# Optimization experiments

Hardware: AMD Instinct MI355X
Metric: run time of the kernel (lower is better)

The kernel has to match this reference:

```python
import jax, jax.numpy as jnp
import numpy as np
from jax import lax

EPS = 1e-5
NBIT = 127.0  # 8-bit symmetric: 2^(8-1)-1

def ste_round(x):
    return x + lax.stop_gradient(jnp.round(x) - x)

def quant_act(x, rng_max):
    # symmetric fake-quant of activations with learned per-cluster range
    s = rng_max / NBIT
    xq = jnp.clip(ste_round(x / s), -NBIT, NBIT) * s
    return xq, s

def fold_bn(w, gamma, beta, mean, var):
    std = jnp.sqrt(var + EPS)
    scale = gamma / std
    w_f = w * scale[:, None, None, None]
    b_f = beta - mean * scale
    return w_f, b_f

def quant_weight(w):
    # per-output-channel symmetric quant
    s = jnp.max(jnp.abs(w), axis=(1, 2, 3), keepdims=True) / NBIT
    wq = jnp.clip(ste_round(w / s), -NBIT, NBIT) * s
    return wq, s.reshape(-1)

def conv(x, w, stride=1, groups=1, pad=0):
    return lax.conv_general_dilated(
        x, w, window_strides=(stride, stride),
        padding=((pad, pad), (pad, pad)),
        dimension_numbers=('NCHW', 'OIHW', 'NCHW'),
        feature_group_count=groups)

def setup_inputs() -> dict:
    key = jax.random.key(0)
    ks = jax.random.split(key, 24)
    B, Cin, H, W = 64, 96, 28, 28
    Cmid, Cout, NC = 576, 96, 4
    d = {}
    d['x'] = jax.random.normal(ks[0], (B, Cin, H, W), dtype=jnp.float32)
    # conv1: 1x1 expansion
    d['w1'] = jax.random.normal(ks[1], (Cmid, Cin, 1, 1), jnp.float32) * 0.1
    d['g1'] = jax.random.uniform(ks[2], (Cmid,), minval=0.5, maxval=1.5)
    d['b1'] = jax.random.normal(ks[3], (Cmid,)) * 0.1
    d['m1'] = jax.random.normal(ks[4], (Cmid,)) * 0.1
    d['v1'] = jax.random.uniform(ks[5], (Cmid,), minval=0.5, maxval=1.5)
    # conv2: 3x3 depthwise
    d['w2'] = jax.random.normal(ks[6], (Cmid, 1, 3, 3), jnp.float32) * 0.1
    d['g2'] = jax.random.uniform(ks[7], (Cmid,), minval=0.5, maxval=1.5)
    d['b2'] = jax.random.normal(ks[8], (Cmid,)) * 0.1
    d['m2'] = jax.random.normal(ks[9], (Cmid,)) * 0.1
    d['v2'] = jax.random.uniform(ks[10], (Cmid,), minval=0.5, maxval=1.5)
    # conv3: 1x1 projection
    d['w3'] = jax.random.normal(ks[11], (Cout, Cmid, 1, 1), jnp.float32) * 0.1
    d['g3'] = jax.random.uniform(ks[12], (Cout,), minval=0.5, maxval=1.5)
    d['b3'] = jax.random.normal(ks[13], (Cout,)) * 0.1
    d['m3'] = jax.random.normal(ks[14], (Cout,)) * 0.1
    d['v3'] = jax.random.uniform(ks[15], (Cout,), minval=0.5, maxval=1.5)
    # per-cluster learned activation ranges for the 4 QuantAct modules
    d['r0'] = jax.random.uniform(ks[16], (NC,), minval=2.0, maxval=8.0)
    d['r1'] = jax.random.uniform(ks[17], (NC,), minval=2.0, maxval=8.0)
    d['r2'] = jax.random.uniform(ks[18], (NC,), minval=2.0, maxval=8.0)
    d['r3'] = jax.random.uniform(ks[19], (NC,), minval=2.0, maxval=8.0)
    d['cluster'] = 2
    return d

def reference(x, w1, g1, b1, m1, v1, w2, g2, b2, m2, v2,
              w3, g3, b3, m3, v3, r0, r1, r2, r3, cluster):
    identity = x  # residual path (in==out, stride==1)
    # QuantAct -> conv1 (BN-folded, per-channel quant) -> ReLU6
    xq, s0 = quant_act(x, r0[cluster])
    w1f, bf1 = fold_bn(w1, g1, b1, m1, v1)
    w1q, ws1 = quant_weight(w1f)
    y = conv(xq, w1q) + bf1[None, :, None, None]
    y = jnp.clip(y, 0.0, 6.0)
    # QuantAct1 -> depthwise conv2 -> ReLU6
    yq, s1 = quant_act(y, r1[cluster])
    w2f, bf2 = fold_bn(w2, g2, b2, m2, v2)
    w2q, ws2 = quant_weight(w2f)
    y = conv(yq, w2q, stride=1, groups=w2.shape[0], pad=1) + bf2[None, :, None, None]
    y = jnp.clip(y, 0.0, 6.0)
    # QuantAct2 -> conv3 projection
    yq, s2 = quant_act(y, r2[cluster])
    w3f, bf3 = fold_bn(w3, g3, b3, m3, v3)
    w3q, ws3 = quant_weight(w3f)
    y = conv(yq, w3q) + bf3[None, :, None, None]
    # residual add, then int32 requant
    y = y + identity
    out, s3 = quant_act(y, r3[cluster])
    return out, s3
```

## Files before the change

kernel.cpp:

```cpp
#include <hip/hip_runtime.h>
#include <cstdint>
#include <cstddef>

typedef int   v4i __attribute__((ext_vector_type(4)));
typedef float v4f __attribute__((ext_vector_type(4)));
typedef unsigned int u32;

constexpr int B_   = 64;
constexpr int CIN  = 96;
constexpr int P_   = 784;
constexpr int CMID = 576;
constexpr int COUT = 96;
constexpr int NOUT = B_ * COUT * P_;
constexpr float NBITF = 127.0f;
constexpr float EPSF  = 1e-5f;
constexpr float MAGICF = 12582912.0f;
constexpr int   BIASI  = 0x4B400000;

constexpr int XB4 = 13 * 8 * 64;
constexpr int YB4 = 13 * 36 * 64;

__device__ __forceinline__ int dot3(u32 a, u32 w, int acc) {
#if __has_builtin(__builtin_amdgcn_sdot4)
    return __builtin_amdgcn_sdot4((int)a, (int)w, acc, false);
#else
    return acc + (int)(signed char)(a)        * (int)(signed char)(w)
               + (int)(signed char)(a >> 8)   * (int)(signed char)(w >> 8)
               + (int)(signed char)(a >> 16)  * (int)(signed char)(w >> 16);
#endif
}

__device__ __forceinline__ void tr4(u32 S0, u32 S1, u32 S2, u32 S3, u32 O[4]) {
    u32 u01 = __builtin_amdgcn_perm(S1, S0, 0x05010400u);
    u32 u23 = __builtin_amdgcn_perm(S3, S2, 0x05010400u);
    u32 v01 = __builtin_amdgcn_perm(S1, S0, 0x07030602u);
    u32 v23 = __builtin_amdgcn_perm(S3, S2, 0x07030602u);
    O[0] = __builtin_amdgcn_perm(u23, u01, 0x05040100u);
    O[1] = __builtin_amdgcn_perm(u23, u01, 0x07060302u);
    O[2] = __builtin_amdgcn_perm(v23, v01, 0x05040100u);
    O[3] = __builtin_amdgcn_perm(v23, v01, 0x07060302u);
}

__device__ __forceinline__ u32 pack4(u32 t0, u32 t1, u32 t2, u32 t3) {
    u32 p01 = __builtin_amdgcn_perm(t1, t0, 0x05010400u);
    u32 p23 = __builtin_amdgcn_perm(t3, t2, 0x05010400u);
    return __builtin_amdgcn_perm(p23, p01, 0x05040100u);
}

__global__ __launch_bounds__(256)
void prep_all(const float* __restrict__ x,
              const float* __restrict__ w1, const float* __restrict__ g1,
              const float* __restrict__ b1, const float* __restrict__ m1,
              const float* __restrict__ v1,
              const float* __restrict__ w2, const float* __restrict__ g2,
              const float* __restrict__ b2, const float* __restrict__ m2,
              const float* __restrict__ v2,
              const float* __restrict__ w3, const float* __restrict__ g3,
              const float* __restrict__ b3, const float* __restrict__ m3,
              const float* __restrict__ v3,
              const float* __restrict__ r0, const float* __restrict__ r1,
              const float* __restrict__ r2, const int* __restrict__ cluster,
              u32* __restrict__ x8t2,
              int8_t* __restrict__ w1qp, float2* __restrict__ e1,
              v4i* __restrict__ w2pk,    float2* __restrict__ e2,
              int8_t* __restrict__ w3qp, float2* __restrict__ e3)
{
    __shared__ u32 T[112 * 37];
    int tid = threadIdx.x;
    int c = cluster[0];

    if (blockIdx.x < 448) {
        int pt0 = blockIdx.x % 7, b = blockIdx.x / 7;
        float inv_s0 = NBITF / r0[c];

        for (int i = tid; i < 112 * 8; i += 256) {
            int row = i >> 3, cc = 24 + (i & 7);
            T[row * 37 + cc] = 0u;
        }
        for (int u = tid; u < 24 * 28; u += 256) {
            int pq = u % 28, icq = u / 28;
            int pxb = pt0 * 112 + pq * 4;
            int q[4][4];
            #pragma unroll
            for (int j = 0; j < 4; j++) {
                v4f xv = *(const v4f*)(x + ((size_t)b * CIN + icq * 4 + j) * P_ + pxb);
                #pragma unroll
                for (int i = 0; i < 4; i++)
                    q[j][i] = (int)fminf(fmaxf(rintf(xv[i] * inv_s0), -127.f), 127.f);
            }
            #pragma unroll
            for (int i = 0; i < 4; i++) {
                u32 t0 = __builtin_amdgcn_perm((u32)q[1][i], (u32)q[0][i], 0x00000400u);
                u32 t1 = __builtin_amdgcn_perm((u32)q[3][i], (u32)q[2][i], 0x00000400u);
                T[(pq * 4 + i) * 37 + icq] = __builtin_amdgcn_perm(t1, t0, 0x05040100u);
            }
        }
        __syncthreads();
        u32* gb = x8t2 + (size_t)b * XB4 * 4;
        for (int i = tid; i < 32 * 112; i += 256) {
            int icq = i / 112, pxo = i - icq * 112;
            int px = pt0 * 112 + pxo;
            gb[(((px >> 6) * 8 + (icq >> 2)) * 64 + (px & 63)) * 4 + (icq & 3)] =
                T[pxo * 37 + icq];
        }
        return;
    }

    int lane = tid & 63, wv = tid >> 6;
    int blk = (blockIdx.x - 448) * 4 + wv;

    const float *w, *g, *bb, *mm, *vv;
    int oc, K, which;
    if (blk < CMID)            { which = 0; w = w1; g = g1; bb = b1; mm = m1; vv = v1; oc = blk;            K = CIN;  }
    else if (blk < 2 * CMID)   { which = 1; w = w2; g = g2; bb = b2; mm = m2; vv = v2; oc = blk - CMID;     K = 9;    }
    else                       { which = 2; w = w3; g = g3; bb = b3; mm = m3; vv = v3; oc = blk - 2 * CMID; K = CMID; }

    float scale = g[oc] / sqrtf(vv[oc] + EPSF);

    float mx = 0.f;
    for (int k = lane; k < K; k += 64)
        mx = fmaxf(mx, fabsf(w[oc * K + k] * scale));
    #pragma unroll
    for (int off = 1; off < 64; off <<= 1)
        mx = fmaxf(mx, __shfl_xor(mx, off));

    float s = mx / NBITF;

    int myq = 0;
    for (int k = lane; k < K; k += 64) {
        float wf = w[oc * K + k] * scale;
        float q  = fminf(fmaxf(rintf(wf / s), -127.f), 127.f);
        if (which == 0)      w1qp[oc * 144 + k] = (int8_t)q;
        else if (which == 1) myq = (int)q;
        else                 w3qp[oc * 592 + k] = (int8_t)q;
    }
    if (which == 0 && lane < 12)
        ((u32*)(w1qp + oc * 144))[24 + lane] = 0u;
    if (which == 1) {
        u32 qq[9];
        #pragma unroll
        for (int t = 0; t < 9; t++) qq[t] = (u32)__shfl(myq, t, 64) & 0xffu;
        if (lane == 0) {
            v4i pk;
            pk[0] = (int)(qq[0] | (qq[1] << 8) | (qq[2] << 16));
            pk[1] = (int)(qq[3] | (qq[4] << 8) | (qq[5] << 16));
            pk[2] = (int)(qq[6] | (qq[7] << 8) | (qq[8] << 16));
            pk[3] = 0;
            w2pk[oc] = pk;
        }
    }
    if (lane == 0) {
        float bf = bb[oc] - mm[oc] * scale;
        float s0 = r0[c] / NBITF, s1 = r1[c] / NBITF, s2 = r2[c] / NBITF;
        if (which == 0) {
            float inv_s1 = NBITF / r1[c];
            e1[oc] = make_float2(s0 * s * inv_s1, bf * inv_s1);
        } else if (which == 1) {
            float inv_s2 = NBITF / r2[c];
            e2[oc] = make_float2(s1 * s * inv_s2, bf * inv_s2);
        } else {
            e3[oc] = make_float2(s2 * s, bf);
        }
    }
}

__global__ __launch_bounds__(256)
void conv12v3(const v4i* __restrict__ x8t2, const v4i* __restrict__ w1q4,
              const float2* __restrict__ e1,
              const v4i* __restrict__ w2pk, const float2* __restrict__ e2,
              const float* __restrict__ r1, const float* __restrict__ r2,
              const int* __restrict__ cluster, v4i* __restrict__ y2t)
{
    __shared__ u32 pool[112 * 36];
    __shared__ u32 y1w[192 * 29];

    int tid = threadIdx.x, b = blockIdx.y;
    int mt = blockIdx.x / 14, rt = blockIdx.x - mt * 14;
    int R0 = 2 * rt;
    int W0 = (R0 - 1) * 28;
    int lane = tid & 63, wv = tid >> 6;
    int n = lane & 15, q4 = lane >> 4;
    int ocw = mt * 192 + wv * 48;

    int c   = cluster[0];
    int u1i = (int)fminf(rintf(6.f * NBITF / r1[c]), 127.f);
    int u2i = (int)fminf(rintf(6.f * NBITF / r2[c]), 127.f);

    const v4i* xb = x8t2 + (size_t)b * XB4;
    for (int u = tid; u < 896; u += 256) {
        int g = u / 112, pxl = u - g * 112;
        int px = min(max(W0 + pxl, 0), P_ - 1);
        v4i v = xb[((px >> 6) * 8 + g) * 64 + (px & 63)];
        *(v4i*)&pool[pxl * 36 + 4 * g] = v;
    }
    __syncthreads();

    #pragma unroll
    for (int jn = 0; jn < 3; jn++) {
        int oc  = ocw + 16 * jn + n;
        int chl = wv * 48 + 16 * jn + n;

        v4i acc[7];
        #pragma unroll
        for (int jm = 0; jm < 7; jm++) acc[jm] = (v4i){0, 0, 0, 0};

        #pragma unroll
        for (int ks = 0; ks < 2; ks++) {
            v4i bw = w1q4[oc * 9 + 4 * ks + q4];
            int g4 = (4 * ks + q4) * 4;
            #pragma unroll
            for (int jm = 0; jm < 7; jm++) {
                v4i af = *(const v4i*)&pool[(16 * jm + n) * 36 + g4];
                acc[jm] = __builtin_amdgcn_mfma_i32_16x16x64_i8(af, bw, acc[jm], 0, 0, 0);
            }
        }

        float2 e = e1[oc];
        #pragma unroll
        for (int jm = 0; jm < 7; jm++) {
            u32 t[4];
            #pragma unroll
            for (int r = 0; r < 4; r++) {
                float f = fmaf((float)acc[jm][r], e.x, e.y) + MAGICF;
                t[r] = (u32)min(max(__float_as_int(f), BIASI), BIASI + u1i);
            }
            int dw = 4 * jm + q4;
            u32 pk = pack4(t[0], t[1], t[2], t[3]);
            pk = ((unsigned)(W0 + 4 * dw) < (unsigned)P_) ? pk : 0u;
            y1w[chl * 29 + dw] = pk;
        }
    }
    __syncthreads();

    u32* y2s = pool;
    for (int u = tid; u < 384; u += 256) {
        int chl = u >> 1, orow = u & 1;
        int ch  = mt * 192 + chl;
        int rb  = chl * 29 + orow * 7;

        v4i wpk = w2pk[ch];
        u32 pk0 = (u32)wpk[0], pk1 = (u32)wpk[1], pk2 = (u32)wpk[2];
        float2 e = e2[ch];

        u32 M0 = 0, M1 = 0, M2 = 0;
        u32 D0 = y1w[rb], D1 = y1w[rb + 7], D2 = y1w[rb + 14];
        #pragma unroll
        for (int xq = 0; xq < 7; xq++) {
            u32 N0, N1, N2;
            if (xq < 6) {
                N0 = y1w[rb + xq + 1];
                N1 = y1w[rb + 7 + xq + 1];
                N2 = y1w[rb + 14 + xq + 1];
            } else { N0 = N1 = N2 = 0u; }

            int a0, a1, a2, a3;
            a0 = dot3(__builtin_amdgcn_alignbyte(D0, M0, 3), pk0, 0);
            a0 = dot3(__builtin_amdgcn_alignbyte(D1, M1, 3), pk1, a0);
            a0 = dot3(__builtin_amdgcn_alignbyte(D2, M2, 3), pk2, a0);
            a1 = dot3(D0, pk0, 0);
            a1 = dot3(D1, pk1, a1);
            a1 = dot3(D2, pk2, a1);
            a2 = dot3(__builtin_amdgcn_alignbyte(N0, D0, 1), pk0, 0);
            a2 = dot3(__builtin_amdgcn_alignbyte(N1, D1, 1), pk1, a2);
            a2 = dot3(__builtin_amdgcn_alignbyte(N2, D2, 1), pk2, a2);
            a3 = dot3(__builtin_amdgcn_alignbyte(N0, D0, 2), pk0, 0);
            a3 = dot3(__builtin_amdgcn_alignbyte(N1, D1, 2), pk1, a3);
            a3 = dot3(__builtin_amdgcn_alignbyte(N2, D2, 2), pk2, a3);

            int aa[4] = {a0, a1, a2, a3};
            u32 tq[4];
            #pragma unroll
            for (int i = 0; i < 4; i++) {
                float f = fmaf((float)aa[i], e.x, e.y) + MAGICF;
                tq[i] = (u32)min(max(__float_as_int(f), BIASI), BIASI + u2i);
            }
            y2s[chl * 15 + orow * 7 + xq] = pack4(tq[0], tq[1], tq[2], tq[3]);

            M0 = D0; M1 = D1; M2 = D2;
            D0 = N0; D1 = N1; D2 = N2;
        }
    }
    __syncthreads();

    v4i* yb = y2t + (size_t)b * YB4;
    for (int u = tid; u < 168; u += 256) {
        int kgl = u / 14, d = u - kgl * 14;
        u32 O[4][4];
        #pragma unroll
        for (int j = 0; j < 4; j++) {
            int cb = (16 * kgl + 4 * j) * 15 + d;
            tr4(y2s[cb], y2s[cb + 15], y2s[cb + 30], y2s[cb + 45], O[j]);
        }
        int gpx0 = R0 * 28 + 4 * d;
        #pragma unroll
        for (int i = 0; i < 4; i++) {
            int gp = gpx0 + i;
            v4i val = (v4i){(int)O[0][i], (int)O[1][i], (int)O[2][i], (int)O[3][i]};
            yb[((gp >> 6) * 36 + mt * 12 + kgl) * 64 + (gp & 63)] = val;
        }
    }
}

__global__ __launch_bounds__(256)
void conv3d(const v4i* __restrict__ y2t, const int8_t* __restrict__ w3qp,
            const float2* __restrict__ e3, const float* __restrict__ x,
            const float* __restrict__ r3, const int* __restrict__ cluster,
            float* __restrict__ out)
{
    int tid = threadIdx.x, b = blockIdx.y, pt = blockIdx.x;
    int lane = tid & 63, wv = tid >> 6;
    int n = lane & 15, q4 = lane >> 4;
    int pxl = wv * 16 + n;
    int px  = pt * 64 + pxl;
    int pxc = min(px, P_ - 1);

    int   c      = cluster[0];
    float s3     = r3[c] / NBITF;
    float inv_s3 = NBITF / r3[c];

    const v4i* yb  = y2t + (size_t)b * YB4;
    int pb3 = (pxc >> 6) * (36 * 64) + (pxc & 63);
    const v4i* w34 = (const v4i*)w3qp;

    v4i acc[6];
    #pragma unroll
    for (int i = 0; i < 6; i++) acc[i] = (v4i){0, 0, 0, 0};

    #pragma unroll
    for (int ks = 0; ks < 9; ks++) {
        v4i bfr = yb[pb3 + (4 * ks + q4) * 64];
        #pragma unroll
        for (int i = 0; i < 6; i++) {
            v4i afr = w34[(i * 16 + n) * 37 + 4 * ks + q4];
            acc[i] = __builtin_amdgcn_mfma_i32_16x16x64_i8(afr, bfr, acc[i], 0, 0, 0);
        }
    }

    if (px < P_) {
        #pragma unroll
        for (int i = 0; i < 6; i++) {
            #pragma unroll
            for (int r = 0; r < 4; r++) {
                int    oc = i * 16 + q4 * 4 + r;
                float2 e  = e3[oc];
                size_t gi = (size_t)(b * COUT + oc) * P_ + px;
                float v  = fmaf((float)acc[i][r], e.x, e.y) + x[gi];
                float f  = fmaf(v, inv_s3, MAGICF);
                int lvl  = min(max(__float_as_int(f) - BIASI, -127), 127);
                out[gi]  = (float)lvl * s3;
            }
        }
    }
    if (pt == 0 && b == 0 && tid == 0)
        out[NOUT] = s3;
}

extern "C" void kernel_launch(void* const* d_in, const int* in_sizes, int n_in,
                              void* d_out, int out_size, void* d_ws, size_t ws_size,
                              hipStream_t stream)
{
    const float* x  = (const float*)d_in[0];
    const float* w1 = (const float*)d_in[1];
    const float* g1 = (const float*)d_in[2];
    const float* b1 = (const float*)d_in[3];
    const float* m1 = (const float*)d_in[4];
    const float* v1 = (const float*)d_in[5];
    const float* w2 = (const float*)d_in[6];
    const float* g2 = (const float*)d_in[7];
    const float* b2 = (const float*)d_in[8];
    const float* m2 = (const float*)d_in[9];
    const float* v2 = (const float*)d_in[10];
    const float* w3 = (const float*)d_in[11];
    const float* g3 = (const float*)d_in[12];
    const float* b3 = (const float*)d_in[13];
    const float* m3 = (const float*)d_in[14];
    const float* v3 = (const float*)d_in[15];
    const float* r0 = (const float*)d_in[16];
    const float* r1 = (const float*)d_in[17];
    const float* r2 = (const float*)d_in[18];
    const float* r3 = (const float*)d_in[19];
    const int*   cl = (const int*)d_in[20];

    float* out = (float*)d_out;

    char*  ws  = (char*)d_ws;
    size_t off = 0;
    auto carve = [&](size_t bytes) {
        size_t cur = off;
        off = (off + bytes + 255) & ~(size_t)255;
        return (void*)(ws + cur);
    };
    int8_t* w1qp = (int8_t*)carve((size_t)CMID * 144);
    float2* e1   = (float2*)carve((size_t)CMID * 8);
    v4i*    w2pk = (v4i*)carve((size_t)CMID * 16);
    float2* e2   = (float2*)carve((size_t)CMID * 8);
    int8_t* w3qp = (int8_t*)carve((size_t)COUT * 592);
    float2* e3   = (float2*)carve((size_t)COUT * 8);
    u32*    x8t2 = (u32*)carve((size_t)B_ * XB4 * 16);
    v4i*    y2t  = (v4i*)carve((size_t)B_ * YB4 * 16);
    (void)ws_size; (void)in_sizes; (void)n_in; (void)out_size;

    prep_all<<<dim3(760), dim3(256), 0, stream>>>(
        x, w1, g1, b1, m1, v1, w2, g2, b2, m2, v2, w3, g3, b3, m3, v3,
        r0, r1, r2, cl, x8t2,
        w1qp, e1, w2pk, e2, w3qp, e3);

    conv12v3<<<dim3(42, B_), dim3(256), 0, stream>>>(
        (const v4i*)x8t2, (const v4i*)w1qp, e1, w2pk, e2, r1, r2, cl, y2t);

    conv3d<<<dim3(13, B_), dim3(256), 0, stream>>>(
        y2t, w3qp, e3, x, r3, cl, out);
}
```

Baseline: 174.7 us.

## Make conv1→depthwise→transpose wave-private to drop block barriers

Restructures the fused conv1/depthwise kernel so each wavefront owns its 48 channels end to end, with private LDS slices for the conv1 output and the depthwise output. This removes two block-wide __syncthreads and replaces the 256-thread strided loops with per-wave lane loops. It also reorders the MFMA loop to iterate pixels outer and channels inner, using a single accumulator per tile, and lays out the x tile as channel-group planes. The catch is more total LDS and lower lane utilisation in the depthwise and transpose stages (96 and 42 items per wave).

```diff
diff --git a/kernel.cpp b/kernel.cpp
--- a/kernel.cpp
+++ b/kernel.cpp
@@ -165,14 +165,15 @@
 }
 
 __global__ __launch_bounds__(256)
-void conv12v3(const v4i* __restrict__ x8t2, const v4i* __restrict__ w1q4,
-              const float2* __restrict__ e1,
-              const v4i* __restrict__ w2pk, const float2* __restrict__ e2,
-              const float* __restrict__ r1, const float* __restrict__ r2,
-              const int* __restrict__ cluster, v4i* __restrict__ y2t)
+void conv12w(const v4i* __restrict__ x8t2, const v4i* __restrict__ w1q4,
+             const float2* __restrict__ e1,
+             const v4i* __restrict__ w2pk, const float2* __restrict__ e2,
+             const float* __restrict__ r1, const float* __restrict__ r2,
+             const int* __restrict__ cluster, v4i* __restrict__ y2t)
 {
-    __shared__ u32 pool[112 * 36];
-    __shared__ u32 y1w[192 * 29];
+    __shared__ v4i xs4[8 * 112];
+    __shared__ u32 y1w[4][48 * 29];
+    __shared__ u32 y2s[4][48 * 15];
 
     int tid = threadIdx.x, b = blockIdx.y;
     int mt = blockIdx.x / 14, rt = blockIdx.x - mt * 14;
@@ -190,52 +191,51 @@
     for (int u = tid; u < 896; u += 256) {
         int g = u / 112, pxl = u - g * 112;
         int px = min(max(W0 + pxl, 0), P_ - 1);
-        v4i v = xb[((px >> 6) * 8 + g) * 64 + (px & 63)];
-        *(v4i*)&pool[pxl * 36 + 4 * g] = v;
+        xs4[g * 112 + pxl] = xb[((px >> 6) * 8 + g) * 64 + (px & 63)];
     }
     __syncthreads();
 
+    u32* myY1 = y1w[wv];
+    u32* myY2 = y2s[wv];
+
+    v4i    bw[3][2];
+    float2 ee[3];
     #pragma unroll
     for (int jn = 0; jn < 3; jn++) {
-        int oc  = ocw + 16 * jn + n;
-        int chl = wv * 48 + 16 * jn + n;
-
-        v4i acc[7];
-        #pragma unroll
-        for (int jm = 0; jm < 7; jm++) acc[jm] = (v4i){0, 0, 0, 0};
-
-        #pragma unroll
-        for (int ks = 0; ks < 2; ks++) {
-            v4i bw = w1q4[oc * 9 + 4 * ks + q4];
-            int g4 = (4 * ks + q4) * 4;
-            #pragma unroll
-            for (int jm = 0; jm < 7; jm++) {
-                v4i af = *(const v4i*)&pool[(16 * jm + n) * 36 + g4];
-                acc[jm] = __builtin_amdgcn_mfma_i32_16x16x64_i8(af, bw, acc[jm], 0, 0, 0);
-            }
-        }
-
-        float2 e = e1[oc];
-        #pragma unroll
-        for (int jm = 0; jm < 7; jm++) {
+        int oc = ocw + 16 * jn + n;
+        bw[jn][0] = w1q4[oc * 9 + q4];
+        bw[jn][1] = w1q4[oc * 9 + 4 + q4];
+        ee[jn] = e1[oc];
+    }
+
+    #pragma unroll
+    for (int jm = 0; jm < 7; jm++) {
+        v4i af0 = xs4[q4 * 112 + 16 * jm + n];
+        v4i af1 = xs4[(4 + q4) * 112 + 16 * jm + n];
+
+        int dw = 4 * jm + q4;
+        bool valid = (unsigned)(W0 + 4 * dw) < (unsigned)P_;
+
+        #pragma unroll
+        for (int jn = 0; jn < 3; jn++) {
+            v4i acc = (v4i){0, 0, 0, 0};
+            acc = __builtin_amdgcn_mfma_i32_16x16x64_i8(af0, bw[jn][0], acc, 0, 0, 0);
+            acc = __builtin_amdgcn_mfma_i32_16x16x64_i8(af1, bw[jn][1], acc, 0, 0, 0);
+
             u32 t[4];
             #pragma unroll
             for (int r = 0; r < 4; r++) {
-                float f = fmaf((float)acc[jm][r], e.x, e.y) + MAGICF;
+                float f = fmaf((float)acc[r], ee[jn].x, ee[jn].y) + MAGICF;
                 t[r] = (u32)min(max(__float_as_int(f), BIASI), BIASI + u1i);
             }
-            int dw = 4 * jm + q4;
             u32 pk = pack4(t[0], t[1], t[2], t[3]);
-            pk = ((unsigned)(W0 + 4 * dw) < (unsigned)P_) ? pk : 0u;
-            y1w[chl * 29 + dw] = pk;
-        }
-    }
-    __syncthreads();
-
-    u32* y2s = pool;
-    for (int u = tid; u < 384; u += 256) {
+            myY1[(16 * jn + n) * 29 + dw] = valid ? pk : 0u;
+        }
+    }
+
+    for (int u = lane; u < 96; u += 64) {
         int chl = u >> 1, orow = u & 1;
-        int ch  = mt * 192 + chl;
+        int ch  = ocw + chl;
         int rb  = chl * 29 + orow * 7;
 
         v4i wpk = w2pk[ch];
@@ -243,14 +243,14 @@
         float2 e = e2[ch];
 
         u32 M0 = 0, M1 = 0, M2 = 0;
-        u32 D0 = y1w[rb], D1 = y1w[rb + 7], D2 = y1w[rb + 14];
+        u32 D0 = myY1[rb], D1 = myY1[rb + 7], D2 = myY1[rb + 14];
         #pragma unroll
         for (int xq = 0; xq < 7; xq++) {
             u32 N0, N1, N2;
             if (xq < 6) {
-                N0 = y1w[rb + xq + 1];
-                N1 = y1w[rb + 7 + xq + 1];
-                N2 = y1w[rb + 14 + xq + 1];
+                N0 = myY1[rb + xq + 1];
+                N1 = myY1[rb + 7 + xq + 1];
+                N2 = myY1[rb + 14 + xq + 1];
             } else { N0 = N1 = N2 = 0u; }
 
             int a0, a1, a2, a3;
@@ -274,29 +274,29 @@
                 float f = fmaf((float)aa[i], e.x, e.y) + MAGICF;
                 tq[i] = (u32)min(max(__float_as_int(f), BIASI), BIASI + u2i);
             }
-            y2s[chl * 15 + orow * 7 + xq] = pack4(tq[0], tq[1], tq[2], tq[3]);
+            myY2[chl * 15 + orow * 7 + xq] = pack4(tq[0], tq[1], tq[2], tq[3]);
 
             M0 = D0; M1 = D1; M2 = D2;
             D0 = N0; D1 = N1; D2 = N2;
         }
     }
-    __syncthreads();
 
     v4i* yb = y2t + (size_t)b * YB4;
-    for (int u = tid; u < 168; u += 256) {
-        int kgl = u / 14, d = u - kgl * 14;
+    if (lane < 42) {
+        int kgl = lane / 14, d = lane - kgl * 14;
         u32 O[4][4];
         #pragma unroll
         for (int j = 0; j < 4; j++) {
             int cb = (16 * kgl + 4 * j) * 15 + d;
-            tr4(y2s[cb], y2s[cb + 15], y2s[cb + 30], y2s[cb + 45], O[j]);
-        }
+            tr4(myY2[cb], myY2[cb + 15], myY2[cb + 30], myY2[cb + 45], O[j]);
+        }
+        int kgG = mt * 12 + wv * 3 + kgl;
         int gpx0 = R0 * 28 + 4 * d;
         #pragma unroll
         for (int i = 0; i < 4; i++) {
             int gp = gpx0 + i;
             v4i val = (v4i){(int)O[0][i], (int)O[1][i], (int)O[2][i], (int)O[3][i]};
-            yb[((gp >> 6) * 36 + mt * 12 + kgl) * 64 + (gp & 63)] = val;
+            yb[((gp >> 6) * 36 + kgG) * 64 + (gp & 63)] = val;
         }
     }
 }
@@ -405,7 +405,7 @@
         r0, r1, r2, cl, x8t2,
         w1qp, e1, w2pk, e2, w3qp, e3);
 
-    conv12v3<<<dim3(42, B_), dim3(256), 0, stream>>>(
+    conv12w<<<dim3(42, B_), dim3(256), 0, stream>>>(
         (const v4i*)x8t2, (const v4i*)w1qp, e1, w2pk, e2, r1, r2, cl, y2t);
 
     conv3d<<<dim3(13, B_), dim3(256), 0, stream>>>(
```

After: 169.1 us. -3.2%, faster.
